# Performance work log

Hardware: AMD Instinct MI355X
Metric: run time of the kernel (lower is better)

The kernel has to match this reference:

```python
import jax, jax.numpy as jnp
import numpy as np

N_HEADS = 16
HEAD_SIZE = 64
N_EMBD = N_HEADS * HEAD_SIZE  # 1024
B, T = 4, 2048


def setup_inputs() -> dict:
    key = jax.random.key(0)
    kx, kq, kk, kv, kp = jax.random.split(key, 5)
    s = 1.0 / np.sqrt(N_EMBD)
    return {
        "x": jax.random.normal(kx, (B, T, N_EMBD), dtype=jnp.float32),
        "Wq": jax.random.normal(kq, (N_EMBD, N_HEADS * HEAD_SIZE), dtype=jnp.float32) * s,
        "Wk": jax.random.normal(kk, (N_EMBD, N_HEADS * HEAD_SIZE), dtype=jnp.float32) * s,
        "Wv": jax.random.normal(kv, (N_EMBD, N_HEADS * HEAD_SIZE), dtype=jnp.float32) * s,
        "Wp": jax.random.normal(kp, (N_HEADS * HEAD_SIZE, N_EMBD), dtype=jnp.float32) * s,
    }


def reference(x, Wq, Wk, Wv, Wp):
    Bb, Tt, C = x.shape
    H, hs = N_HEADS, HEAD_SIZE
    # QKV projections (no bias), split heads: (B, H, T, hs)
    q = (x @ Wq).reshape(Bb, Tt, H, hs).transpose(0, 2, 1, 3)
    k = (x @ Wk).reshape(Bb, Tt, H, hs).transpose(0, 2, 1, 3)
    v = (x @ Wv).reshape(Bb, Tt, H, hs).transpose(0, 2, 1, 3)
    scores = jnp.einsum("bhqd,bhkd->bhqk", q, k) / np.sqrt(hs).astype(np.float32)
    causal = jnp.tril(jnp.ones((Tt, Tt), dtype=bool))
    scores = jnp.where(causal, scores, -jnp.inf)
    attn = jax.nn.softmax(scores, axis=-1)  # dropout p=0 -> identity
    o = jnp.einsum("bhqk,bhkd->bhqd", attn, v)  # (B, H, T, hs)
    # Faithfully replicate torch's view/transpose/view sequence:
    o = o.reshape(Bb, Tt, H * hs)          # raw reshape of (B,H,T,hs) buffer
    o = jnp.swapaxes(o, 1, 2)               # (B, H*hs, T)
    o = o.reshape(Bb, Tt, H * hs)           # contiguous().view
    return o @ Wp
```

## Files before the change

### kernel.cpp

```cpp
#include <hip/hip_runtime.h>

typedef unsigned short ush;
typedef unsigned int u32;
typedef __attribute__((ext_vector_type(4))) float f32x4;
typedef __attribute__((ext_vector_type(8))) short short8;
typedef __attribute__((ext_vector_type(8))) ush ushx8;
typedef __attribute__((ext_vector_type(4))) ush ushx4;

#define GAS __attribute__((address_space(1)))
#define LAS __attribute__((address_space(3)))

__device__ __forceinline__ void gl_lds16(const void* g, void* l) {
  __builtin_amdgcn_global_load_lds((const GAS void*)g, (LAS void*)l, 16, 0, 0);
}

__device__ __forceinline__ ush f2bf(float f) {
  union { float f; unsigned int u; } x; x.f = f;
  unsigned int r = x.u + 0x7fffu + ((x.u >> 16) & 1u);
  return (ush)(r >> 16);
}
__device__ __forceinline__ u32 fbits(float f) {
  union { float f; u32 u; } x; x.f = f; return x.u;
}

#define NEG_BIG (-1.0e4f)
#define SCL 0.18033688f

__global__ __launch_bounds__(256) void k_convert_x(
    const float* __restrict__ X, ush* __restrict__ Xb) {
  int idx = blockIdx.x * 256 + threadIdx.x;
  int base = idx * 8;
  f32x4 a = *(const f32x4*)(X + base);
  f32x4 b = *(const f32x4*)(X + base + 4);
  ushx8 o;
#pragma unroll
  for (int q = 0; q < 4; ++q) { o[q] = f2bf(a[q]); o[4 + q] = f2bf(b[q]); }
  *(ushx8*)(Xb + base) = o;
}

__global__ __launch_bounds__(256) void k_transpose_w(
    const float* __restrict__ W0, const float* __restrict__ W1,
    const float* __restrict__ W2, const float* __restrict__ W3,
    ush* __restrict__ Wt) {
  __shared__ ush Ts[64][72];
  const int z = blockIdx.z;
  const float* W = (z == 0) ? W0 : (z == 1) ? W1 : (z == 2) ? W2 : W3;
  ush* Ot = Wt + (size_t)z * 1048576;
  const int k0 = blockIdx.x * 64, n0 = blockIdx.y * 64;
  const int rr = threadIdx.x >> 4, cc = threadIdx.x & 15;
#pragma unroll
  for (int i = 0; i < 4; ++i) {
    int row = i * 16 + rr;
    f32x4 v = *(const f32x4*)(W + (size_t)(k0 + row) * 1024 + n0 + cc * 4);
#pragma unroll
    for (int q = 0; q < 4; ++q) Ts[row][cc * 4 + q] = f2bf(v[q]);
  }
  __syncthreads();
#pragma unroll
  for (int i = 0; i < 4; ++i) {
    int n = i * 16 + rr;
    ushx4 o;
#pragma unroll
    for (int q = 0; q < 4; ++q) o[q] = Ts[cc * 4 + q][n];
    *(ushx4*)(Ot + (size_t)(n0 + n) * 1024 + k0 + cc * 4) = o;
  }
}

__global__ __launch_bounds__(512, 2) void k_gemm_qkv(
    const ush* __restrict__ X, const ush* __restrict__ Wt, ush* __restrict__ QKV) {
  __shared__ __align__(16) ush As_[2][16384];
  __shared__ __align__(16) ush Bs_[2][8192];
  const int tid = threadIdx.x;
  const int w = tid >> 6, l = tid & 63, lr = l & 15, lg = l >> 4;
  const int wm = w >> 2, wn = w & 3;
  const int mt = blockIdx.x, nt = blockIdx.y;
  const int which = nt >> 3, n0 = (nt & 7) * 128;
  const ush* Ag = X + (size_t)mt * 256 * 1024;
  const ush* Bg = Wt + (size_t)which * 1048576 + (size_t)n0 * 1024;
  int aoff[4], boff[2];
#pragma unroll
  for (int it = 0; it < 4; ++it) {
    int ch = it * 512 + tid, row = ch >> 3, g = ch & 7;
    aoff[it] = row * 1024 + ((g ^ (row & 7)) << 3);
  }
#pragma unroll
  for (int it = 0; it < 2; ++it) {
    int ch = it * 512 + tid, row = ch >> 3, g = ch & 7;
    boff[it] = row * 1024 + ((g ^ (row & 7)) << 3);
  }
  f32x4 acc[8][2] = {};

  auto issueS = [&](int kt, int buf) {
    const ush* Asrc = Ag + kt * 64;
    const ush* Bsrc = Bg + kt * 64;
#pragma unroll
    for (int it = 0; it < 4; ++it)
      gl_lds16(Asrc + aoff[it], &As_[buf][((size_t)it * 512 + tid) * 8]);
#pragma unroll
    for (int it = 0; it < 2; ++it)
      gl_lds16(Bsrc + boff[it], &Bs_[buf][((size_t)it * 512 + tid) * 8]);
  };

  issueS(0, 0);
  for (int t = 0; t < 16; ++t) {
    if (t < 15) {
      issueS(t + 1, (t + 1) & 1);
      asm volatile("s_waitcnt vmcnt(6)" ::: "memory");
    } else {
      asm volatile("s_waitcnt vmcnt(0)" ::: "memory");
    }
    __syncthreads();
    const ush* Ab = As_[t & 1];
    const ush* Bb = Bs_[t & 1];
    short8 fb[2][2];
#pragma unroll
    for (int ni = 0; ni < 2; ++ni)
#pragma unroll
      for (int kk = 0; kk < 2; ++kk) {
        int row = wn * 32 + ni * 16 + lr;
        fb[ni][kk] = *(const short8*)(Bb + row * 64 + (((kk * 4 + lg) ^ (row & 7)) << 3));
      }
#pragma unroll
    for (int qm = 0; qm < 4; ++qm) {
      short8 fa[2][2];
#pragma unroll
      for (int m2 = 0; m2 < 2; ++m2)
#pragma unroll
        for (int kk = 0; kk < 2; ++kk) {
          int row = wm * 128 + (qm * 2 + m2) * 16 + lr;
          fa[m2][kk] = *(const short8*)(Ab + row * 64 + (((kk * 4 + lg) ^ (row & 7)) << 3));
        }
      __builtin_amdgcn_s_setprio(1);
#pragma unroll
      for (int m2 = 0; m2 < 2; ++m2)
#pragma unroll
        for (int ni = 0; ni < 2; ++ni)
#pragma unroll
          for (int kk = 0; kk < 2; ++kk)
            acc[qm * 2 + m2][ni] = __builtin_amdgcn_mfma_f32_16x16x32_bf16(
                fa[m2][kk], fb[ni][kk], acc[qm * 2 + m2][ni], 0, 0, 0);
      __builtin_amdgcn_s_setprio(0);
    }
    __syncthreads();
  }
  ush* Ct = &As_[0][0];
#pragma unroll
  for (int mi = 0; mi < 8; ++mi)
#pragma unroll
    for (int ni = 0; ni < 2; ++ni)
#pragma unroll
      for (int j = 0; j < 4; ++j)
        Ct[(wm * 128 + mi * 16 + lg * 4 + j) * 128 + wn * 32 + ni * 16 + lr] =
            f2bf(acc[mi][ni][j]);
  __syncthreads();
  ush* Om = QKV + (size_t)which * 8388608;
  const int m0 = mt * 256, b = m0 >> 11, t0 = m0 & 2047, h0 = n0 >> 6;
#pragma unroll
  for (int it = 0; it < 8; ++it) {
    int c = it * 512 + tid;
    int hsel = c >> 11;
    int cc = c & 2047;
    int r = cc >> 3;
    int c8 = (cc & 7) * 8;
    ushx8 v = *(const ushx8*)(Ct + r * 128 + hsel * 64 + c8);
    *(ushx8*)(Om + ((size_t)(b * 16 + h0 + hsel) * 2048 + t0 + r) * 64 + c8) = v;
  }
}

__global__ __launch_bounds__(256) void k_transpose_v(
    const ush* __restrict__ V, ush* __restrict__ Vt) {
  __shared__ ush Ts[64][66];
  const int tt = blockIdx.x, bh = blockIdx.y;
  const ush* Vh = V + (size_t)bh * 131072 + tt * 4096;
  ush* Oh = Vt + (size_t)bh * 131072 + tt * 64;
  const int tid = threadIdx.x;
#pragma unroll
  for (int it = 0; it < 2; ++it) {
    int idx = it * 256 + tid;
    int row = idx >> 3, c8 = (idx & 7) * 8;
    ushx8 v = *(const ushx8*)(Vh + row * 64 + c8);
#pragma unroll
    for (int k2 = 0; k2 < 8; ++k2) Ts[row][c8 + k2] = v[k2];
  }
  __syncthreads();
#pragma unroll
  for (int it = 0; it < 2; ++it) {
    int idx = it * 256 + tid;
    int d = idx >> 3, c8 = (idx & 7) * 8;
    ushx8 o;
#pragma unroll
    for (int k2 = 0; k2 < 8; ++k2) o[k2] = Ts[c8 + k2][d];
    *(ushx8*)(Oh + (size_t)d * 2048 + c8) = o;
  }
}

__global__ __launch_bounds__(256) void k_attn(
    const ush* __restrict__ Q, const ush* __restrict__ K,
    const ush* __restrict__ Vg, ush* __restrict__ O) {
  __shared__ __align__(16) ush Ks[2][4096];
  __shared__ __align__(16) ush Vs[2][4096];
  __shared__ __align__(16) ush Pl[8][1024];
  const int lid = blockIdx.x + 16 * blockIdx.y;
  const int qta = (lid >> 3) & 15;
  const int bh  = ((lid >> 7) << 3) | (lid & 7);
  const int qtb = 31 - qta;
  const size_t hb = (size_t)bh * (2048 * 64);
  const ush* Qh = Q + hb;
  const ush* Kh = K + hb;
  const ush* Vh = Vg + hb;
  const int tid = threadIdx.x, w = tid >> 6, l = tid & 63, lr = l & 15, lg = l >> 4;
  const int q0a = qta * 64 + w * 16, q0b = qtb * 64 + w * 16;

  short8 qfa[2], qfb[2];
#pragma unroll
  for (int s = 0; s < 2; ++s) {
    qfa[s] = *(const short8*)(Qh + (size_t)(q0a + lr) * 64 + s * 32 + lg * 8);
    qfb[s] = *(const short8*)(Qh + (size_t)(q0b + lr) * 64 + s * 32 + lg * 8);
  }
  f32x4 acca[4] = {}, accb[4] = {};
  float la[4] = {0.f, 0.f, 0.f, 0.f}, lb[4] = {0.f, 0.f, 0.f, 0.f};

  int koff[2], voff[2];
#pragma unroll
  for (int it = 0; it < 2; ++it) {
    int ch = it * 256 + tid;
    int r = ch >> 3, g = ch & 7;
    koff[it] = r * 64 + ((g ^ (r & 7)) << 3);
    int keyv = ((r & 7) + (r >> 3)) & 7;
    voff[it] = r * 2048 + ((g ^ keyv) << 3);
  }
  auto issueStage = [&](int c, int buf) {
#pragma unroll
    for (int it = 0; it < 2; ++it) {
      int ch = it * 256 + tid;
      gl_lds16(Kh + (size_t)c * 4096 + koff[it], &Ks[buf][ch * 8]);
      gl_lds16(Vh + c * 64 + voff[it], &Vs[buf][ch * 8]);
    }
  };

  auto ctile = [&](const ush* Kc, const ush* Vc, const short8* qf,
                   f32x4* acc, float* lrow, bool diag, ush* PlW) {
    f32x4 sf[4] = {};
#pragma unroll
    for (int s = 0; s < 2; ++s)
#pragma unroll
      for (int f = 0; f < 4; ++f) {
        int kv = f * 16 + lr;
        short8 kf = *(const short8*)(Kc + kv * 64 + (((s * 4 + lg) ^ (kv & 7)) << 3));
        sf[f] = __builtin_amdgcn_mfma_f32_16x16x32_bf16(qf[s], kf, sf[f], 0, 0, 0);
      }
#pragma unroll
    for (int f = 0; f < 4; ++f)
#pragma unroll
      for (int j = 0; j < 4; ++j) {
        float vv = sf[f][j] * SCL;
        if (diag && (f * 16 + lr) > (w * 16 + lg * 4 + j)) vv = NEG_BIG;
        sf[f][j] = __builtin_amdgcn_exp2f(vv);
      }
#pragma unroll
    for (int j = 0; j < 4; ++j)
      lrow[j] += (sf[0][j] + sf[1][j]) + (sf[2][j] + sf[3][j]);
#pragma unroll
    for (int f = 0; f < 4; ++f)
#pragma unroll
      for (int j = 0; j < 4; ++j) {
        int q = lg * 4 + j;
        PlW[q * 64 + ((f * 16 + lr) ^ ((q & 7) << 3))] = (ush)(fbits(sf[f][j]) >> 16);
      }
#pragma unroll
    for (int s = 0; s < 2; ++s) {
      short8 pf = *(const short8*)(PlW + lr * 64 + (((s * 4 + lg) ^ (lr & 7)) << 3));
#pragma unroll
      for (int db = 0; db < 4; ++db) {
        int dv = db * 16 + lr;
        int keyv = ((dv & 7) + (dv >> 3)) & 7;
        short8 vf = *(const short8*)(Vc + dv * 64 + (((s * 4 + lg) ^ keyv) << 3));
        acc[db] = __builtin_amdgcn_mfma_f32_16x16x32_bf16(pf, vf, acc[db], 0, 0, 0);
      }
    }
  };

  issueStage(0, 0);
  int cur = 0;
  for (int c = 0; c <= qtb; ++c) {
    asm volatile("s_waitcnt vmcnt(0)" ::: "memory");
    __syncthreads();
    if (c < qtb) issueStage(c + 1, cur ^ 1);
    const ush* Kc = Ks[cur];
    const ush* Vc = Vs[cur];
    if (c <= qta) ctile(Kc, Vc, qfa, acca, la, c == qta, Pl[w]);
    ctile(Kc, Vc, qfb, accb, lb, c == qtb, Pl[4 + w]);
    __syncthreads();
    cur ^= 1;
  }

#pragma unroll
  for (int msk = 1; msk <= 8; msk <<= 1)
#pragma unroll
    for (int j = 0; j < 4; ++j) {
      la[j] += __shfl_xor(la[j], msk);
      lb[j] += __shfl_xor(lb[j], msk);
    }
  float ia[4], ib[4];
#pragma unroll
  for (int j = 0; j < 4; ++j) {
    ia[j] = __builtin_amdgcn_rcpf(la[j]);
    ib[j] = __builtin_amdgcn_rcpf(lb[j]);
  }
  ush* Oh = O + hb;
#pragma unroll
  for (int db = 0; db < 4; ++db)
#pragma unroll
    for (int j = 0; j < 4; ++j) {
      Oh[(size_t)(q0a + lg * 4 + j) * 64 + db * 16 + lr] = f2bf(acca[db][j] * ia[j]);
      Oh[(size_t)(q0b + lg * 4 + j) * 64 + db * 16 + lr] = f2bf(accb[db][j] * ib[j]);
    }
}

__global__ __launch_bounds__(256) void k_gather(const ush* __restrict__ Ob, ush* __restrict__ Mb) {
  __shared__ ush Ls[2][128][68];
  const int jh = blockIdx.x, tau = blockIdx.y, b = blockIdx.z;
  const int tid = threadIdx.x;
#pragma unroll
  for (int it = 0; it < 8; ++it) {
    int c = it * 256 + tid;
    int r = c >> 3, d8 = (c & 7) * 8;
    int esel = r >> 7, jlow = r & 127;
    ushx8 v = *(const ushx8*)(Ob +
        ((size_t)(b * 16 + jh + esel * 8) * 2048 + jlow * 16 + tau) * 64 + d8);
    *(ushx8*)(&Ls[esel][jlow][d8]) = v;
  }
  __syncthreads();
  const int wv = tid >> 6, l = tid & 63;
  const int e = wv >> 1, jhalf = wv & 1, d = l;
  ush* Mrow = Mb + (size_t)b * 2097152 +
              (size_t)(128 * tau + 2 * d + e) * 1024 + jh * 128 + jhalf * 64;
#pragma unroll
  for (int ch = 0; ch < 8; ++ch) {
    ushx8 v;
#pragma unroll
    for (int k = 0; k < 8; ++k) v[k] = Ls[e][jhalf * 64 + ch * 8 + k][d];
    *(ushx8*)(Mrow + ch * 8) = v;
  }
}

__global__ __launch_bounds__(512, 2) void k_gemm_out(
    const ush* __restrict__ A, const ush* __restrict__ Bt, float* __restrict__ Out) {
  __shared__ __align__(16) ush As_[2][16384];
  __shared__ __align__(16) ush Bs_[2][8192];
  const int tid = threadIdx.x;
  const int w = tid >> 6, l = tid & 63, lr = l & 15, lg = l >> 4;
  const int wm = w >> 2, wn = w & 3;
  const int mt = blockIdx.x, nt = blockIdx.y;
  const int n0 = nt * 128;
  const ush* Ag = A + (size_t)mt * 256 * 1024;
  const ush* Bg = Bt + (size_t)n0 * 1024;
  int aoff[4], boff[2];
#pragma unroll
  for (int it = 0; it < 4; ++it) {
    int ch = it * 512 + tid, row = ch >> 3, g = ch & 7;
    aoff[it] = row * 1024 + ((g ^ (row & 7)) << 3);
  }
#pragma unroll
  for (int it = 0; it < 2; ++it) {
    int ch = it * 512 + tid, row = ch >> 3, g = ch & 7;
    boff[it] = row * 1024 + ((g ^ (row & 7)) << 3);
  }
  f32x4 acc[8][2] = {};

  auto issueS = [&](int kt, int buf) {
    const ush* Asrc = Ag + kt * 64;
    const ush* Bsrc = Bg + kt * 64;
#pragma unroll
    for (int it = 0; it < 4; ++it)
      gl_lds16(Asrc + aoff[it], &As_[buf][((size_t)it * 512 + tid) * 8]);
#pragma unroll
    for (int it = 0; it < 2; ++it)
      gl_lds16(Bsrc + boff[it], &Bs_[buf][((size_t)it * 512 + tid) * 8]);
  };

  issueS(0, 0);
  for (int t = 0; t < 16; ++t) {
    if (t < 15) {
      issueS(t + 1, (t + 1) & 1);
      asm volatile("s_waitcnt vmcnt(6)" ::: "memory");
    } else {
      asm volatile("s_waitcnt vmcnt(0)" ::: "memory");
    }
    __syncthreads();
    const ush* Ab = As_[t & 1];
    const ush* Bb = Bs_[t & 1];
    short8 fb[2][2];
#pragma unroll
    for (int ni = 0; ni < 2; ++ni)
#pragma unroll
      for (int kk = 0; kk < 2; ++kk) {
        int row = wn * 32 + ni * 16 + lr;
        fb[ni][kk] = *(const short8*)(Bb + row * 64 + (((kk * 4 + lg) ^ (row & 7)) << 3));
      }
#pragma unroll
    for (int qm = 0; qm < 4; ++qm) {
      short8 fa[2][2];
#pragma unroll
      for (int m2 = 0; m2 < 2; ++m2)
#pragma unroll
        for (int kk = 0; kk < 2; ++kk) {
          int row = wm * 128 + (qm * 2 + m2) * 16 + lr;
          fa[m2][kk] = *(const short8*)(Ab + row * 64 + (((kk * 4 + lg) ^ (row & 7)) << 3));
        }
      __builtin_amdgcn_s_setprio(1);
#pragma unroll
      for (int m2 = 0; m2 < 2; ++m2)
#pragma unroll
        for (int ni = 0; ni < 2; ++ni)
#pragma unroll
          for (int kk = 0; kk < 2; ++kk)
            acc[qm * 2 + m2][ni] = __builtin_amdgcn_mfma_f32_16x16x32_bf16(
                fa[m2][kk], fb[ni][kk], acc[qm * 2 + m2][ni], 0, 0, 0);
      __builtin_amdgcn_s_setprio(0);
    }
    __syncthreads();
  }
  const int m0 = mt * 256;
#pragma unroll
  for (int mi = 0; mi < 8; ++mi)
#pragma unroll
    for (int ni = 0; ni < 2; ++ni)
#pragma unroll
      for (int j = 0; j < 4; ++j)
        Out[(size_t)(m0 + wm * 128 + mi * 16 + lg * 4 + j) * 1024 +
            n0 + wn * 32 + ni * 16 + lr] = acc[mi][ni][j];
}

extern "C" void kernel_launch(void* const* d_in, const int* in_sizes, int n_in,
                              void* d_out, int out_size, void* d_ws, size_t ws_size,
                              hipStream_t stream) {
  const float* x  = (const float*)d_in[0];
  const float* wq = (const float*)d_in[1];
  const float* wk = (const float*)d_in[2];
  const float* wv = (const float*)d_in[3];
  const float* wp = (const float*)d_in[4];
  float* out = (float*)d_out;
  char* ws = (char*)d_ws;
  ush* xb  = (ush*)ws;
  ush* wt  = (ush*)(ws + 16777216);
  ush* qkv = (ush*)(ws + 25165824);
  ush* vtg = xb;
  ush* ob  = qkv;
  ush* mb  = xb;

  k_convert_x<<<dim3(4096), 256, 0, stream>>>(x, xb);
  k_transpose_w<<<dim3(16, 16, 4), 256, 0, stream>>>(wq, wk, wv, wp, wt);
  k_gemm_qkv<<<dim3(32, 24), 512, 0, stream>>>(xb, wt, qkv);
  k_transpose_v<<<dim3(32, 64), 256, 0, stream>>>(qkv + 16777216, vtg);
  k_attn<<<dim3(16, 64), 256, 0, stream>>>(qkv, qkv + 8388608, vtg, ob);
  k_gather<<<dim3(8, 16, 4), 256, 0, stream>>>(ob, mb);
  k_gemm_out<<<dim3(32, 8), 512, 0, stream>>>(mb, wt + 3145728, out);
}
```

Before: 215.2 us.

## Fuse prep kernels, write transposed V from QKV GEMM, drop attn barrier

Merges the x conversion and weight transpose into a single prep launch, and has the QKV GEMM epilogue write V directly in transposed layout into a separate workspace region, which removes the standalone V-transpose kernel. It also removes the trailing __syncthreads in the attention loop. The goal is fewer launches and one less full pass over V through memory. The transposed V store reads LDS column-wise, which may cause bank conflicts. The remaining barrier at the top of the next iteration appears to still protect buffer reuse, but the barrier removal could race if prefetch of stage c+1 overwrites data still being read.

```diff
diff --git a/kernel.cpp b/kernel.cpp
--- a/kernel.cpp
+++ b/kernel.cpp
@@ -26,27 +26,28 @@
 #define NEG_BIG (-1.0e4f)
 #define SCL 0.18033688f
 
-__global__ __launch_bounds__(256) void k_convert_x(
-    const float* __restrict__ X, ush* __restrict__ Xb) {
-  int idx = blockIdx.x * 256 + threadIdx.x;
-  int base = idx * 8;
-  f32x4 a = *(const f32x4*)(X + base);
-  f32x4 b = *(const f32x4*)(X + base + 4);
-  ushx8 o;
-#pragma unroll
-  for (int q = 0; q < 4; ++q) { o[q] = f2bf(a[q]); o[4 + q] = f2bf(b[q]); }
-  *(ushx8*)(Xb + base) = o;
-}
-
-__global__ __launch_bounds__(256) void k_transpose_w(
-    const float* __restrict__ W0, const float* __restrict__ W1,
-    const float* __restrict__ W2, const float* __restrict__ W3,
-    ush* __restrict__ Wt) {
+__global__ __launch_bounds__(256) void k_prep(
+    const float* __restrict__ X, const float* __restrict__ W0,
+    const float* __restrict__ W1, const float* __restrict__ W2,
+    const float* __restrict__ W3, ush* __restrict__ Xb, ush* __restrict__ Wt) {
   __shared__ ush Ts[64][72];
-  const int z = blockIdx.z;
+  const int bx = blockIdx.x;
+  if (bx < 4096) {
+    int idx = bx * 256 + threadIdx.x;
+    int base = idx * 8;
+    f32x4 a = *(const f32x4*)(X + base);
+    f32x4 b = *(const f32x4*)(X + base + 4);
+    ushx8 o;
+#pragma unroll
+    for (int q = 0; q < 4; ++q) { o[q] = f2bf(a[q]); o[4 + q] = f2bf(b[q]); }
+    *(ushx8*)(Xb + base) = o;
+    return;
+  }
+  const int bid = bx - 4096;
+  const int z = bid >> 8;
+  const int k0 = (bid & 15) * 64, n0 = ((bid >> 4) & 15) * 64;
   const float* W = (z == 0) ? W0 : (z == 1) ? W1 : (z == 2) ? W2 : W3;
   ush* Ot = Wt + (size_t)z * 1048576;
-  const int k0 = blockIdx.x * 64, n0 = blockIdx.y * 64;
   const int rr = threadIdx.x >> 4, cc = threadIdx.x & 15;
 #pragma unroll
   for (int i = 0; i < 4; ++i) {
@@ -67,7 +68,8 @@
 }
 
 __global__ __launch_bounds__(512, 2) void k_gemm_qkv(
-    const ush* __restrict__ X, const ush* __restrict__ Wt, ush* __restrict__ QKV) {
+    const ush* __restrict__ X, const ush* __restrict__ Wt,
+    ush* __restrict__ QKV, ush* __restrict__ Vtg) {
   __shared__ __align__(16) ush As_[2][16384];
   __shared__ __align__(16) ush Bs_[2][8192];
   const int tid = threadIdx.x;
@@ -153,44 +155,31 @@
         Ct[(wm * 128 + mi * 16 + lg * 4 + j) * 128 + wn * 32 + ni * 16 + lr] =
             f2bf(acc[mi][ni][j]);
   __syncthreads();
-  ush* Om = QKV + (size_t)which * 8388608;
   const int m0 = mt * 256, b = m0 >> 11, t0 = m0 & 2047, h0 = n0 >> 6;
-#pragma unroll
-  for (int it = 0; it < 8; ++it) {
-    int c = it * 512 + tid;
-    int hsel = c >> 11;
-    int cc = c & 2047;
-    int r = cc >> 3;
-    int c8 = (cc & 7) * 8;
-    ushx8 v = *(const ushx8*)(Ct + r * 128 + hsel * 64 + c8);
-    *(ushx8*)(Om + ((size_t)(b * 16 + h0 + hsel) * 2048 + t0 + r) * 64 + c8) = v;
-  }
-}
-
-__global__ __launch_bounds__(256) void k_transpose_v(
-    const ush* __restrict__ V, ush* __restrict__ Vt) {
-  __shared__ ush Ts[64][66];
-  const int tt = blockIdx.x, bh = blockIdx.y;
-  const ush* Vh = V + (size_t)bh * 131072 + tt * 4096;
-  ush* Oh = Vt + (size_t)bh * 131072 + tt * 64;
-  const int tid = threadIdx.x;
-#pragma unroll
-  for (int it = 0; it < 2; ++it) {
-    int idx = it * 256 + tid;
-    int row = idx >> 3, c8 = (idx & 7) * 8;
-    ushx8 v = *(const ushx8*)(Vh + row * 64 + c8);
-#pragma unroll
-    for (int k2 = 0; k2 < 8; ++k2) Ts[row][c8 + k2] = v[k2];
-  }
-  __syncthreads();
-#pragma unroll
-  for (int it = 0; it < 2; ++it) {
-    int idx = it * 256 + tid;
-    int d = idx >> 3, c8 = (idx & 7) * 8;
-    ushx8 o;
-#pragma unroll
-    for (int k2 = 0; k2 < 8; ++k2) o[k2] = Ts[c8 + k2][d];
-    *(ushx8*)(Oh + (size_t)d * 2048 + c8) = o;
+  if (which == 2) {
+    const int cc = tid & 127, rq = tid >> 7;
+    const int hsel = cc >> 6, d = cc & 63;
+    ush* dst = Vtg + (size_t)(b * 16 + h0 + hsel) * 131072 + (size_t)d * 2048 +
+               t0 + rq * 64;
+#pragma unroll
+    for (int ch = 0; ch < 8; ++ch) {
+      ushx8 v;
+#pragma unroll
+      for (int k = 0; k < 8; ++k) v[k] = Ct[(rq * 64 + ch * 8 + k) * 128 + cc];
+      *(ushx8*)(dst + ch * 8) = v;
+    }
+  } else {
+    ush* Om = QKV + (size_t)which * 8388608;
+#pragma unroll
+    for (int it = 0; it < 8; ++it) {
+      int c = it * 512 + tid;
+      int hsel = c >> 11;
+      int cc = c & 2047;
+      int r = cc >> 3;
+      int c8 = (cc & 7) * 8;
+      ushx8 v = *(const ushx8*)(Ct + r * 128 + hsel * 64 + c8);
+      *(ushx8*)(Om + ((size_t)(b * 16 + h0 + hsel) * 2048 + t0 + r) * 64 + c8) = v;
+    }
   }
 }
 
@@ -290,7 +279,6 @@
     const ush* Vc = Vs[cur];
     if (c <= qta) ctile(Kc, Vc, qfa, acca, la, c == qta, Pl[w]);
     ctile(Kc, Vc, qfb, accb, lb, c == qtb, Pl[4 + w]);
-    __syncthreads();
     cur ^= 1;
   }
 
@@ -445,14 +433,12 @@
   ush* xb  = (ush*)ws;
   ush* wt  = (ush*)(ws + 16777216);
   ush* qkv = (ush*)(ws + 25165824);
-  ush* vtg = xb;
+  ush* vtg = (ush*)(ws + 75497472);
   ush* ob  = qkv;
   ush* mb  = xb;
 
-  k_convert_x<<<dim3(4096), 256, 0, stream>>>(x, xb);
-  k_transpose_w<<<dim3(16, 16, 4), 256, 0, stream>>>(wq, wk, wv, wp, wt);
-  k_gemm_qkv<<<dim3(32, 24), 512, 0, stream>>>(xb, wt, qkv);
-  k_transpose_v<<<dim3(32, 64), 256, 0, stream>>>(qkv + 16777216, vtg);
+  k_prep<<<dim3(5120), 256, 0, stream>>>(x, wq, wk, wv, wp, xb, wt);
+  k_gemm_qkv<<<dim3(32, 24), 512, 0, stream>>>(xb, wt, qkv, vtg);
   k_attn<<<dim3(16, 64), 256, 0, stream>>>(qkv, qkv + 8388608, vtg, ob);
   k_gather<<<dim3(8, 16, 4), 256, 0, stream>>>(ob, mb);
   k_gemm_out<<<dim3(32, 8), 512, 0, stream>>>(mb, wt + 3145728, out);
```

Result: faster. 206.7 us (-3.9%).
